# Kernel tuning notes

Hardware: AMD Instinct MI355X
Metric: run time of the kernel (lower is better)

## Reference

```python
import jax, jax.numpy as jnp
import numpy as np

HEADS = 4
DIM_HEAD = 32
EPS = 1e-5


def setup_inputs() -> dict:
    key = jax.random.key(0)
    ks = jax.random.split(key, 4)
    B, dim, H, W = 8, 256, 128, 128
    hidden = HEADS * DIM_HEAD  # 128
    x = jax.random.normal(ks[0], (B, dim, H, W), dtype=jnp.float32)
    # 1x1 conv weights stored as [out_ch, in_ch]
    qkv_w = jax.random.normal(ks[1], (3 * hidden, dim), dtype=jnp.float32) * (1.0 / np.sqrt(dim))
    conv_w = jax.random.normal(ks[2], (dim, hidden), dtype=jnp.float32) * (1.0 / np.sqrt(hidden))
    conv_b = jax.random.normal(ks[3], (dim,), dtype=jnp.float32) * 0.01
    gamma = jnp.ones((dim,), dtype=jnp.float32)
    beta = jnp.zeros((dim,), dtype=jnp.float32)
    return {"x": x, "qkv_w": qkv_w, "conv_w": conv_w, "conv_b": conv_b,
            "gamma": gamma, "beta": beta}


def reference(x, qkv_w, conv_w, conv_b, gamma, beta):
    B, C, H, W = x.shape
    N = H * W
    scale = DIM_HEAD ** (-0.5)
    # qkv 1x1 conv -> [B, 3, heads, dim_head, N]
    qkv = jnp.einsum('oc,bchw->bohw', qkv_w, x).reshape(B, 3, HEADS, DIM_HEAD, N)
    q, k, v = qkv[:, 0], qkv[:, 1], qkv[:, 2]
    q = jax.nn.softmax(q, axis=-2) * scale   # softmax over dim_head axis
    k = jax.nn.softmax(k, axis=-1)           # softmax over spatial axis
    v = v / N
    # context = k @ v^T : [B, h, d, d]
    context = jnp.einsum('bhdn,bhen->bhde', k, v)
    # out = context @ q : [B, h, d, N]
    out = jnp.einsum('bhde,bhen->bhdn', context, q)
    out = out.reshape(B, HEADS * DIM_HEAD, H, W)
    # final 1x1 conv with bias
    y = jnp.einsum('oc,bchw->bohw', conv_w, out) + conv_b[None, :, None, None]
    # InstanceNorm2d(affine=True): per-sample per-channel over (H, W), biased var
    mean = jnp.mean(y, axis=(2, 3), keepdims=True)
    var = jnp.var(y, axis=(2, 3), keepdims=True)
    y = (y - mean) * jax.lax.rsqrt(var + EPS)
    return y * gamma[None, :, None, None] + beta[None, :, None, None]
```

## Files before the change

### kernel.cpp

```cpp
#include <hip/hip_runtime.h>
#include <math.h>

#define NPIX 16384
#define DIMC 256
#define BATCH 8
#define HEADS 4
#define DHEAD 32
#define HID 128
#define OQKV 384
#define EPS 1e-5f
#define SCALE 0.17677669529663687f

typedef _Float16 f16x8 __attribute__((ext_vector_type(8)));
typedef _Float16 f16x4 __attribute__((ext_vector_type(4)));
typedef float f32x4 __attribute__((ext_vector_type(4)));

__device__ inline void gl_lds16(const void* g, void* l) {
    __builtin_amdgcn_global_load_lds(
        (const __attribute__((address_space(1))) unsigned*)g,
        (__attribute__((address_space(3))) unsigned*)l, 16, 0, 0);
}

__global__ __launch_bounds__(256) void prep_kernel(
    const float* __restrict__ qkv_w, const float* __restrict__ conv_w,
    _Float16* __restrict__ wh, _Float16* __restrict__ ch, float* __restrict__ zbuf)
{
    int i = blockIdx.x * 256 + threadIdx.x;
    if (i < 98304) wh[i] = (_Float16)qkv_w[i];
    else           ch[i - 98304] = (_Float16)conv_w[i - 98304];
    if (i < 37888) zbuf[i] = 0.f;
}

__global__ __launch_bounds__(256) void gemm_qkv(
    const _Float16* __restrict__ A,
    const float* __restrict__ X,
    _Float16* __restrict__ Cm)
{
    __shared__ _Float16 smem[24576];
    const int t  = threadIdx.x;
    const int b  = blockIdx.x;
    const int m0 = blockIdx.y * 128;
    const int n0 = blockIdx.z * 128;
    const float* Xb = X + (long)b * DIMC * NPIX;
    const int w = t >> 6, lane = t & 63;
    const int q = lane >> 4, l16 = lane & 15;
    const int mw = (w >> 1) * 64, nw = (w & 1) * 64;

    f32x4 acc[4][4] = {};

    auto STAGE = [&](int buf, int k0) {
        _Float16* As = smem + buf * 12288;
        float*    Xs = (float*)(smem + buf * 12288 + 4096);
        #pragma unroll
        for (int is = 0; is < 2; is++) {
            int idx = is * 256 + t;
            int row = idx >> 2, kc = (idx & 3) * 8;
            gl_lds16(&A[(long)(m0 + row) * DIMC + k0 + kc], &As[idx * 8]);
        }
        #pragma unroll
        for (int is = 0; is < 4; is++) {
            int idx = is * 256 + t;
            int c = idx >> 5, f4 = (idx & 31) * 4;
            gl_lds16(&Xb[(long)(k0 + c) * NPIX + n0 + f4], &Xs[c * 128 + f4]);
        }
    };

    STAGE(0, 0);
    __syncthreads();
    int cur = 0;

    for (int kt = 0; kt < 8; kt++) {
        if (kt < 7) STAGE(cur ^ 1, (kt + 1) * 32);

        const _Float16* As = smem + cur * 12288;
        const float*    Xs = (const float*)(smem + cur * 12288 + 4096);

        f16x8 af[4], bf[4];
        #pragma unroll
        for (int i = 0; i < 4; i++)
            af[i] = *(const f16x8*)&As[(mw + i * 16 + l16) * 32 + q * 8];
        #pragma unroll
        for (int kk = 0; kk < 8; kk++) {
            f32x4 xv = *(const f32x4*)&Xs[(q * 8 + kk) * 128 + nw + l16 * 4];
            bf[0][kk] = (_Float16)xv[0];
            bf[1][kk] = (_Float16)xv[1];
            bf[2][kk] = (_Float16)xv[2];
            bf[3][kk] = (_Float16)xv[3];
        }
        #pragma unroll
        for (int i = 0; i < 4; i++)
            #pragma unroll
            for (int j = 0; j < 4; j++)
                acc[i][j] = __builtin_amdgcn_mfma_f32_16x16x32_f16(af[i], bf[j], acc[i][j], 0, 0, 0);

        __builtin_amdgcn_sched_barrier(0);
        asm volatile("s_waitcnt vmcnt(0) lgkmcnt(0)" ::: "memory");
        __builtin_amdgcn_s_barrier();
        cur ^= 1;
    }

    _Float16* Cs = smem;
    #pragma unroll
    for (int i = 0; i < 4; i++) {
        #pragma unroll
        for (int r = 0; r < 4; r++) {
            int row = mw + i * 16 + q * 4 + r;
            int col = nw + l16 * 4;
            f16x4 h4;
            h4[0] = (_Float16)acc[i][0][r];
            h4[1] = (_Float16)acc[i][1][r];
            h4[2] = (_Float16)acc[i][2][r];
            h4[3] = (_Float16)acc[i][3][r];
            *(f16x4*)&Cs[row * 128 + (col ^ ((row & 15) << 3))] = h4;
        }
    }
    __syncthreads();
    _Float16* Cb = Cm + (long)b * ((long)OQKV * NPIX);
    #pragma unroll
    for (int it = 0; it < 8; it++) {
        int u = it * 256 + t;
        int row = u >> 4, cg = u & 15;
        f16x8 v8 = *(const f16x8*)&Cs[row * 128 + ((cg * 8) ^ ((row & 15) << 3))];
        *(f16x8*)&Cb[(long)(m0 + row) * NPIX + n0 + cg * 8] = v8;
    }
}

template<int K, int EPI>
__global__ __launch_bounds__(256) void gemm_h(
    const _Float16* __restrict__ A,
    const _Float16* __restrict__ Bm,
    _Float16* __restrict__ Cm,
    long bsB, long bsC, float* __restrict__ lnacc)
{
    __shared__ _Float16 smem[16384];
    const int t  = threadIdx.x;
    const int b  = blockIdx.x;
    const int m0 = blockIdx.y * 128;
    const int n0 = blockIdx.z * 128;
    const _Float16* Bb = Bm + (long)b * bsB;
    const int w = t >> 6, lane = t & 63;
    const int q = lane >> 4, l16 = lane & 15;
    const int mw = (w >> 1) * 64, nw = (w & 1) * 64;

    f32x4 acc[4][4] = {};

    auto STAGE = [&](int buf, int k0) {
        _Float16* As = smem + buf * 8192;
        _Float16* Bs = smem + buf * 8192 + 4096;
        #pragma unroll
        for (int is = 0; is < 2; is++) {
            int idx = is * 256 + t;
            int row = idx >> 2, kc = (idx & 3) * 8;
            gl_lds16(&A [(long)(m0 + row) * K + k0 + kc], &As[idx * 8]);
            gl_lds16(&Bb[(long)(n0 + row) * K + k0 + kc], &Bs[idx * 8]);
        }
    };

    STAGE(0, 0);
    __syncthreads();
    int cur = 0;
    constexpr int NS = K / 32;

    for (int kt = 0; kt < NS; kt++) {
        if (kt < NS - 1) STAGE(cur ^ 1, (kt + 1) * 32);

        const _Float16* As = smem + cur * 8192;
        const _Float16* Bs = smem + cur * 8192 + 4096;

        f16x8 af[4], bf[4];
        #pragma unroll
        for (int i = 0; i < 4; i++) {
            af[i] = *(const f16x8*)&As[(mw + i * 16 + l16) * 32 + q * 8];
            bf[i] = *(const f16x8*)&Bs[(nw + i * 16 + l16) * 32 + q * 8];
        }
        #pragma unroll
        for (int i = 0; i < 4; i++)
            #pragma unroll
            for (int j = 0; j < 4; j++)
                acc[i][j] = __builtin_amdgcn_mfma_f32_16x16x32_f16(af[i], bf[j], acc[i][j], 0, 0, 0);

        __builtin_amdgcn_sched_barrier(0);
        asm volatile("s_waitcnt vmcnt(0) lgkmcnt(0)" ::: "memory");
        __builtin_amdgcn_s_barrier();
        cur ^= 1;
    }

    _Float16* Cs = smem;
    #pragma unroll
    for (int i = 0; i < 4; i++) {
        #pragma unroll
        for (int j = 0; j < 4; j++) {
            #pragma unroll
            for (int r = 0; r < 4; r++) {
                int row = mw + i * 16 + q * 4 + r;
                int col = nw + j * 16 + l16;
                Cs[row * 128 + (col ^ ((row & 15) << 3))] = (_Float16)acc[i][j][r];
            }
        }
    }
    __syncthreads();
    _Float16* Cb = Cm + (long)b * bsC;
    #pragma unroll
    for (int it = 0; it < 8; it++) {
        int u = it * 256 + t;
        int row = u >> 4, cg = u & 15;
        f16x8 v8 = *(const f16x8*)&Cs[row * 128 + ((cg * 8) ^ ((row & 15) << 3))];
        *(f16x8*)&Cb[(long)(m0 + row) * NPIX + n0 + cg * 8] = v8;
        if (EPI) {
            float s = 0.f, sq = 0.f;
            #pragma unroll
            for (int k = 0; k < 8; k++) { float f = (float)v8[k]; s += f; sq += f * f; }
            #pragma unroll
            for (int off = 8; off > 0; off >>= 1) {
                s  += __shfl_down(s,  off, 16);
                sq += __shfl_down(sq, off, 16);
            }
            if ((t & 15) == 0) {
                int rg = b * DIMC + m0 + row;
                atomicAdd(&lnacc[rg * 2],     s);
                atomicAdd(&lnacc[rg * 2 + 1], sq);
            }
        }
    }
}

__global__ __launch_bounds__(256) void ctx_mfma(const _Float16* __restrict__ qkvh,
    float* __restrict__ ctx_raw, float* __restrict__ ksum)
{
    __shared__ float cbuf[4][1024];
    int t = threadIdx.x;
    int w = t >> 6, lane = t & 63;
    int q = lane >> 4, l16 = lane & 15;
    int bh = blockIdx.y, b = bh >> 2, h = bh & 3;
    const _Float16* kb = qkvh + ((long)b * OQKV + HID + h * DHEAD) * NPIX;
    const _Float16* vb = qkvh + ((long)b * OQKV + 2 * HID + h * DHEAD) * NPIX;
    long n0 = (long)blockIdx.x * 2048 + w * 512 + q * 8;

    f32x4 c00 = {}, c01 = {}, c10 = {}, c11 = {};
    float ks0 = 0.f, ks1 = 0.f;

    for (int s = 0; s < 16; s++) {
        long n = n0 + s * 32;
        f16x8 kf0 = *(const f16x8*)&kb[(long)l16 * NPIX + n];
        f16x8 kf1 = *(const f16x8*)&kb[(long)(16 + l16) * NPIX + n];
        f16x8 vf0 = *(const f16x8*)&vb[(long)l16 * NPIX + n];
        f16x8 vf1 = *(const f16x8*)&vb[(long)(16 + l16) * NPIX + n];
        f16x8 e0, e1;
        #pragma unroll
        for (int j = 0; j < 8; j++) {
            float ea = __expf((float)kf0[j]); e0[j] = (_Float16)ea; ks0 += ea;
            float eb = __expf((float)kf1[j]); e1[j] = (_Float16)eb; ks1 += eb;
        }
        c00 = __builtin_amdgcn_mfma_f32_16x16x32_f16(e0, vf0, c00, 0, 0, 0);
        c01 = __builtin_amdgcn_mfma_f32_16x16x32_f16(e0, vf1, c01, 0, 0, 0);
        c10 = __builtin_amdgcn_mfma_f32_16x16x32_f16(e1, vf0, c10, 0, 0, 0);
        c11 = __builtin_amdgcn_mfma_f32_16x16x32_f16(e1, vf1, c11, 0, 0, 0);
    }

    ks0 += __shfl_down(ks0, 32); ks0 += __shfl_down(ks0, 16);
    ks1 += __shfl_down(ks1, 32); ks1 += __shfl_down(ks1, 16);
    if (lane < 16) {
        atomicAdd(&ksum[bh * DHEAD + l16],      ks0);
        atomicAdd(&ksum[bh * DHEAD + 16 + l16], ks1);
    }

    float* cb = cbuf[w];
    #pragma unroll
    for (int r = 0; r < 4; r++) {
        cb[(q * 4 + r) * 32 + l16]            = c00[r];
        cb[(q * 4 + r) * 32 + 16 + l16]       = c01[r];
        cb[(16 + q * 4 + r) * 32 + l16]       = c10[r];
        cb[(16 + q * 4 + r) * 32 + 16 + l16]  = c11[r];
    }
    __syncthreads();
    #pragma unroll
    for (int ii = 0; ii < 4; ii++) {
        int idx = ii * 256 + t;
        float s = cbuf[0][idx] + cbuf[1][idx] + cbuf[2][idx] + cbuf[3][idx];
        atomicAdd(&ctx_raw[(long)bh * 1024 + idx], s);
    }
}

__global__ __launch_bounds__(256) void outq_h(_Float16* __restrict__ qkvh,
    const float* __restrict__ ctx_raw, const float* __restrict__ ksum)
{
    __shared__ float ctx_t[4][32][32];
    int tid = threadIdx.x;
    int n = blockIdx.x * 256 + tid;
    int b = blockIdx.y;
    #pragma unroll
    for (int i = 0; i < 16; i++) {
        int idx = i * 256 + tid;
        int h = idx >> 10, de = idx & 1023;
        int d = de >> 5, e = de & 31;
        float s = ksum[(b * 4 + h) * DHEAD + d];
        ctx_t[h][e][d] = SCALE * ctx_raw[(long)(b * 4 + h) * 1024 + de] / s;
    }
    __syncthreads();
    _Float16* ob = qkvh + ((long)b * OQKV + 2 * HID) * NPIX + (long)n * HID;
    for (int h = 0; h < 4; h++) {
        const _Float16* qb = qkvh + ((long)b * OQKV + h * DHEAD) * NPIX + n;
        float qv[32];
        float mx = -1e30f;
        #pragma unroll
        for (int e = 0; e < 32; e++) { qv[e] = (float)qb[(long)e * NPIX]; mx = fmaxf(mx, qv[e]); }
        float s = 0.f;
        #pragma unroll
        for (int e = 0; e < 32; e++) { qv[e] = __expf(qv[e] - mx); s += qv[e]; }
        float qs = 1.f / s;
        float4 o4[8];
        #pragma unroll
        for (int j = 0; j < 8; j++) o4[j] = make_float4(0,0,0,0);
        #pragma unroll 8
        for (int e = 0; e < 32; e++) {
            float qe = qv[e] * qs;
            #pragma unroll
            for (int j = 0; j < 8; j++) {
                float4 c = *(const float4*)&ctx_t[h][e][j * 4];
                o4[j].x += c.x * qe; o4[j].y += c.y * qe;
                o4[j].z += c.z * qe; o4[j].w += c.w * qe;
            }
        }
        #pragma unroll
        for (int j = 0; j < 4; j++) {
            f16x8 pk;
            float4 a = o4[j * 2], bb = o4[j * 2 + 1];
            pk[0] = (_Float16)a.x;  pk[1] = (_Float16)a.y;
            pk[2] = (_Float16)a.z;  pk[3] = (_Float16)a.w;
            pk[4] = (_Float16)bb.x; pk[5] = (_Float16)bb.y;
            pk[6] = (_Float16)bb.z; pk[7] = (_Float16)bb.w;
            *(f16x8*)&ob[h * DHEAD + j * 8] = pk;
        }
    }
}

__global__ __launch_bounds__(256) void ln_finalize(const float* __restrict__ lnacc,
    const float* __restrict__ gamma, const float* __restrict__ beta,
    float* __restrict__ mv)
{
    int row = blockIdx.x * 256 + threadIdx.x;
    float s = lnacc[row * 2], sq = lnacc[row * 2 + 1];
    float meanp = s * (1.f / NPIX);
    float varp  = fmaxf(sq * (1.f / NPIX) - meanp * meanp, 0.f);
    float rinv  = rsqrtf(varp * (1.f / ((float)NPIX * (float)NPIX)) + EPS);
    int c = row & 255;
    float g = rinv * gamma[c];
    mv[row * 2]     = g * (1.f / NPIX);
    mv[row * 2 + 1] = beta[c] - meanp * (1.f / NPIX) * g;
}

__global__ __launch_bounds__(256) void ln_apply(const _Float16* __restrict__ yh,
    const float* __restrict__ mv, float* __restrict__ out)
{
    long i8 = (long)blockIdx.x * 256 + threadIdx.x;
    int row = (int)(i8 >> 11);
    float a = mv[row * 2], be = mv[row * 2 + 1];
    f16x8 v = *(const f16x8*)&yh[i8 * 8];
    float4 o1, o2;
    o1.x = (float)v[0] * a + be; o1.y = (float)v[1] * a + be;
    o1.z = (float)v[2] * a + be; o1.w = (float)v[3] * a + be;
    o2.x = (float)v[4] * a + be; o2.y = (float)v[5] * a + be;
    o2.z = (float)v[6] * a + be; o2.w = (float)v[7] * a + be;
    *(float4*)&out[i8 * 8]     = o1;
    *(float4*)&out[i8 * 8 + 4] = o2;
}

extern "C" void kernel_launch(void* const* d_in, const int* in_sizes, int n_in,
                              void* d_out, int out_size, void* d_ws, size_t ws_size,
                              hipStream_t stream)
{
    const float* x      = (const float*)d_in[0];
    const float* qkv_w  = (const float*)d_in[1];
    const float* conv_w = (const float*)d_in[2];
    const float* gamma  = (const float*)d_in[4];
    const float* beta   = (const float*)d_in[5];
    float* out = (float*)d_out;

    _Float16* yh   = (_Float16*)d_ws;
    _Float16* qkvh = yh + 33554432;
    _Float16* wh   = qkvh + 50331648;
    _Float16* ch   = wh + 98304;
    float* ctx_raw = (float*)(ch + 32768);
    float* ksum    = ctx_raw + 32768;
    float* lnacc   = ksum + 1024;
    float* mv      = lnacc + 4096;

    prep_kernel<<<512, 256, 0, stream>>>(qkv_w, conv_w, wh, ch, ctx_raw);
    gemm_qkv<<<dim3(BATCH, 3, 128), 256, 0, stream>>>(wh, x, qkvh);
    ctx_mfma<<<dim3(8, 32), 256, 0, stream>>>(qkvh, ctx_raw, ksum);
    outq_h<<<dim3(64, BATCH), 256, 0, stream>>>(qkvh, ctx_raw, ksum);
    gemm_h<128, 1><<<dim3(BATCH, 2, 128), 256, 0, stream>>>(
        ch, qkvh + (long)2 * HID * NPIX, yh, (long)OQKV * NPIX, (long)DIMC * NPIX, lnacc);
    ln_finalize<<<8, 256, 0, stream>>>(lnacc, gamma, beta, mv);
    ln_apply<<<16384, 256, 0, stream>>>(yh, mv, out);
}
```

Baseline: 377.0 us.

## Load QKV GEMM operands directly from global into registers, dropping LDS staging

```diff
diff --git a/kernel.cpp b/kernel.cpp
--- a/kernel.cpp
+++ b/kernel.cpp
@@ -31,12 +31,12 @@
     if (i < 37888) zbuf[i] = 0.f;
 }
 
-__global__ __launch_bounds__(256) void gemm_qkv(
+__global__ __launch_bounds__(256, 4) void gemm_qkv(
     const _Float16* __restrict__ A,
     const float* __restrict__ X,
     _Float16* __restrict__ Cm)
 {
-    __shared__ _Float16 smem[24576];
+    __shared__ _Float16 Cs[16384];
     const int t  = threadIdx.x;
     const int b  = blockIdx.x;
     const int m0 = blockIdx.y * 128;
@@ -46,60 +46,37 @@
     const int q = lane >> 4, l16 = lane & 15;
     const int mw = (w >> 1) * 64, nw = (w & 1) * 64;
 
+    const _Float16* Ap = A + (long)(m0 + mw + l16) * DIMC + q * 8;
+    const float*    Xp = Xb + (long)(q * 8) * NPIX + n0 + nw + l16 * 4;
+
     f32x4 acc[4][4] = {};
 
-    auto STAGE = [&](int buf, int k0) {
-        _Float16* As = smem + buf * 12288;
-        float*    Xs = (float*)(smem + buf * 12288 + 4096);
-        #pragma unroll
-        for (int is = 0; is < 2; is++) {
-            int idx = is * 256 + t;
-            int row = idx >> 2, kc = (idx & 3) * 8;
-            gl_lds16(&A[(long)(m0 + row) * DIMC + k0 + kc], &As[idx * 8]);
-        }
-        #pragma unroll
-        for (int is = 0; is < 4; is++) {
-            int idx = is * 256 + t;
-            int c = idx >> 5, f4 = (idx & 31) * 4;
-            gl_lds16(&Xb[(long)(k0 + c) * NPIX + n0 + f4], &Xs[c * 128 + f4]);
-        }
-    };
-
-    STAGE(0, 0);
-    __syncthreads();
-    int cur = 0;
-
+    #pragma unroll
     for (int kt = 0; kt < 8; kt++) {
-        if (kt < 7) STAGE(cur ^ 1, (kt + 1) * 32);
-
-        const _Float16* As = smem + cur * 12288;
-        const float*    Xs = (const float*)(smem + cur * 12288 + 4096);
-
-        f16x8 af[4], bf[4];
+        const int k0 = kt * 32;
+        f16x8 af[4];
+        f32x4 xr[8];
         #pragma unroll
         for (int i = 0; i < 4; i++)
-            af[i] = *(const f16x8*)&As[(mw + i * 16 + l16) * 32 + q * 8];
+            af[i] = *(const f16x8*)&Ap[(long)(i * 16) * DIMC + k0];
+        #pragma unroll
+        for (int kk = 0; kk < 8; kk++)
+            xr[kk] = *(const f32x4*)&Xp[(long)(k0 + kk) * NPIX];
+        f16x8 bf[4];
         #pragma unroll
         for (int kk = 0; kk < 8; kk++) {
-            f32x4 xv = *(const f32x4*)&Xs[(q * 8 + kk) * 128 + nw + l16 * 4];
-            bf[0][kk] = (_Float16)xv[0];
-            bf[1][kk] = (_Float16)xv[1];
-            bf[2][kk] = (_Float16)xv[2];
-            bf[3][kk] = (_Float16)xv[3];
+            bf[0][kk] = (_Float16)xr[kk][0];
+            bf[1][kk] = (_Float16)xr[kk][1];
+            bf[2][kk] = (_Float16)xr[kk][2];
+            bf[3][kk] = (_Float16)xr[kk][3];
         }
         #pragma unroll
         for (int i = 0; i < 4; i++)
             #pragma unroll
             for (int j = 0; j < 4; j++)
                 acc[i][j] = __builtin_amdgcn_mfma_f32_16x16x32_f16(af[i], bf[j], acc[i][j], 0, 0, 0);
-
-        __builtin_amdgcn_sched_barrier(0);
-        asm volatile("s_waitcnt vmcnt(0) lgkmcnt(0)" ::: "memory");
-        __builtin_amdgcn_s_barrier();
-        cur ^= 1;
-    }
-
-    _Float16* Cs = smem;
+    }
+
     #pragma unroll
     for (int i = 0; i < 4; i++) {
         #pragma unroll
```

Result: slower. 417.2 us (+10.7%).
